# Optimization experiments

Hardware: AMD Instinct MI355X
Metric: run time of the kernel (lower is better)

The kernel has to match this reference:

```python
import jax, jax.numpy as jnp
import numpy as np

GRID = 7
NUM_CLASSES = 80
LAMBDA_COORD = 5.0
LAMBDA_NOOBJ = 0.5
EPS_IOU = 1e-06
EPS_SQRT = 1e-06


def setup_inputs() -> dict:
    key = jax.random.key(0)
    k1, k2, k3 = jax.random.split(key, 3)
    B = 4096
    D = 10 + NUM_CLASSES
    pred = jax.random.uniform(k1, (B, GRID, GRID, D), dtype=jnp.float32)
    target = jax.random.uniform(k2, (B, GRID, GRID, D), dtype=jnp.float32)
    # confidence channel of target must be exactly 1.0 for object cells
    obj = (jax.random.uniform(k3, (B, GRID, GRID)) < 0.25).astype(jnp.float32)
    target = target.at[..., 4].set(obj)
    return {"pred": pred, "target": target}


def _iou(b1, b2):
    # b1, b2: [..., 4] boxes as (cx, cy, w, h) in image coords
    x1, y1, w1, h1 = b1[..., 0], b1[..., 1], b1[..., 2], b1[..., 3]
    x2, y2, w2, h2 = b2[..., 0], b2[..., 1], b2[..., 2], b2[..., 3]
    ix_min = jnp.maximum(x1 - w1 / 2, x2 - w2 / 2)
    iy_min = jnp.maximum(y1 - h1 / 2, y2 - h2 / 2)
    ix_max = jnp.minimum(x1 + w1 / 2, x2 + w2 / 2)
    iy_max = jnp.minimum(y1 + h1 / 2, y2 + h2 / 2)
    iw = jnp.clip(ix_max - ix_min, 0.0)
    ih = jnp.clip(iy_max - iy_min, 0.0)
    inter = iw * ih
    union = w1 * h1 + w2 * h2 - inter
    return inter / (union + EPS_IOU)


def _forward(pred, target):
    S = pred.shape[1]
    gy = jnp.arange(S, dtype=pred.dtype).reshape(1, S, 1)
    gx = jnp.arange(S, dtype=pred.dtype).reshape(1, 1, S)

    def to_img(box5):  # [B,S,S,5] cell-relative -> [B,S,S,4] image coords
        cx = (gx + box5[..., 0]) / S
        cy = (gy + box5[..., 1]) / S
        return jnp.stack([cx, cy, box5[..., 2], box5[..., 3]], axis=-1)

    box1 = pred[..., 0:5]
    box2 = pred[..., 5:10]
    tbox = target[..., 0:5]

    iou1 = _iou(to_img(box1), to_img(tbox))
    iou2 = _iou(to_img(box2), to_img(tbox))
    resp1 = iou1 > iou2  # box1 responsible if strictly greater (matches `if iou1 > iou2`)
    best = jnp.where(resp1[..., None], box1, box2)  # [B,S,S,5]

    obj = target[..., 4] == 1.0  # [B,S,S]
    objf = obj.astype(pred.dtype)
    n_obj = jnp.sum(objf)
    n_cells = jnp.asarray(pred.shape[0] * S * S, pred.dtype)

    # coord: mean-of-2 xy MSE + mean-of-2 sqrt(wh) MSE per responsible box
    dxy2 = jnp.sum((best[..., 0:2] - tbox[..., 0:2]) ** 2, axis=-1)
    swh_p = jnp.sqrt(jnp.clip(best[..., 2:4], EPS_SQRT))
    swh_t = jnp.sqrt(jnp.clip(tbox[..., 2:4], EPS_SQRT))
    dwh2 = jnp.sum((swh_p - swh_t) ** 2, axis=-1)
    coord_per = 0.5 * dxy2 + 0.5 * dwh2
    coord_loss = jnp.sum(coord_per * objf) / jnp.maximum(n_obj, 1.0)

    # confidence: obj cells -> (best_conf - 1)^2 (count 1); noobj -> lam*(c1^2 + c2^2) (count 2)
    conf_obj = (best[..., 4] - 1.0) ** 2
    conf_noobj = LAMBDA_NOOBJ * (pred[..., 4] ** 2 + pred[..., 9] ** 2)
    conf_sum = jnp.sum(jnp.where(obj, conf_obj, conf_noobj))
    conf_count = n_obj + 2.0 * (n_cells - n_obj)
    conf_loss = conf_sum / jnp.maximum(conf_count, 1.0)

    # class: mean over classes per obj cell
    class_per = jnp.mean((pred[..., 10:] - target[..., 10:]) ** 2, axis=-1)
    class_loss = jnp.sum(class_per * objf) / jnp.maximum(n_obj, 1.0)

    return LAMBDA_COORD * coord_loss + conf_loss + class_loss


def reference(pred, target):
    return _forward(pred, target)
```

## Files before the change

kernel.cpp:

```cpp
#include <hip/hip_runtime.h>

#define GRID_S 7
#define NUM_CLASSES 80
#define D_DIM 90
#define LAMBDA_COORD 5.0f
#define LAMBDA_NOOBJ 0.5f
#define EPS_IOU 1e-6f
#define EPS_SQRT 1e-6f

__device__ __forceinline__ float iou_img(float cx1, float cy1, float w1, float h1,
                                         float cx2, float cy2, float w2, float h2) {
    float ixmin = fmaxf(cx1 - w1 * 0.5f, cx2 - w2 * 0.5f);
    float iymin = fmaxf(cy1 - h1 * 0.5f, cy2 - h2 * 0.5f);
    float ixmax = fminf(cx1 + w1 * 0.5f, cx2 + w2 * 0.5f);
    float iymax = fminf(cy1 + h1 * 0.5f, cy2 + h2 * 0.5f);
    float iw = fmaxf(ixmax - ixmin, 0.0f);
    float ih = fmaxf(iymax - iymin, 0.0f);
    float inter = iw * ih;
    float uni = w1 * h1 + w2 * h2 - inter;
    return inter / (uni + EPS_IOU);
}

__global__ __launch_bounds__(256) void yolo_gated_kernel(
        const float* __restrict__ pred, const float* __restrict__ targ,
        float* __restrict__ part, int ncells) {
    const int tid = threadIdx.x;
    const int cell = blockIdx.x * 256 + tid;

    __shared__ int s_list[256];
    __shared__ int s_count;
    if (tid == 0) s_count = 0;
    __syncthreads();

    float v_obj = 0.0f, v_coord = 0.0f, v_conf = 0.0f, v_cls = 0.0f;

    bool obj = false;
    if (cell < ncells) {
        const float2* t2 = (const float2*)(targ + (size_t)cell * D_DIM);
        const float2* p2 = (const float2*)(pred + (size_t)cell * D_DIM);
        float2 tf = t2[2];
        float2 pa = p2[2];
        float2 pb = p2[4];
        obj = (tf.x == 1.0f);
        if (obj) {
            v_obj = 1.0f;
        } else {
            v_conf = LAMBDA_NOOBJ * (pa.x * pa.x + pb.y * pb.y);
        }
    }

    if (obj) {
        int idx = atomicAdd(&s_count, 1);
        s_list[idx] = cell;
    }
    __syncthreads();
    const int n = s_count;

    const int lane6 = tid & 63;
    const int sub = tid >> 6;
    for (int k0 = 0; k0 < n; k0 += 64) {
        const int k = k0 + lane6;
        if (k < n) {
            const int c = s_list[k];
            const float2* p2 = (const float2*)(pred + (size_t)c * D_DIM);
            const float2* t2 = (const float2*)(targ + (size_t)c * D_DIM);

            float cls0 = 0.0f, cls1 = 0.0f;
            const int s2 = 5 + 10 * sub;
            #pragma unroll
            for (int j = 0; j < 10; ++j) {
                float2 pc = p2[s2 + j];
                float2 tc = t2[s2 + j];
                float dx = pc.x - tc.x;
                float dy = pc.y - tc.y;
                cls0 = fmaf(dx, dx, cls0);
                cls1 = fmaf(dy, dy, cls1);
            }
            v_cls += (cls0 + cls1) * (1.0f / (float)NUM_CLASSES);

            if (sub == 0) {
                float2 pq0 = p2[0], pq1 = p2[1], pq2 = p2[2], pq3 = p2[3], pq4 = p2[4];
                float2 tq0 = t2[0], tq1 = t2[1];

                float b1x = pq0.x, b1y = pq0.y, b1w = pq1.x, b1h = pq1.y, b1c = pq2.x;
                float b2x = pq2.y, b2y = pq3.x, b2w = pq3.y, b2h = pq4.x, b2c = pq4.y;
                float tbx = tq0.x, tby = tq0.y, tbw = tq1.x, tbh = tq1.y;

                const int gxy = c % (GRID_S * GRID_S);
                const float gy = (float)(gxy / GRID_S);
                const float gx = (float)(gxy % GRID_S);
                const float invS = 1.0f / (float)GRID_S;
                float c1x = (gx + b1x) * invS, c1y = (gy + b1y) * invS;
                float c2x = (gx + b2x) * invS, c2y = (gy + b2y) * invS;
                float ctx = (gx + tbx) * invS, cty = (gy + tby) * invS;

                float iou1 = iou_img(c1x, c1y, b1w, b1h, ctx, cty, tbw, tbh);
                float iou2 = iou_img(c2x, c2y, b2w, b2h, ctx, cty, tbw, tbh);
                bool resp1 = iou1 > iou2;

                float bx = resp1 ? b1x : b2x;
                float by = resp1 ? b1y : b2y;
                float bw = resp1 ? b1w : b2w;
                float bh = resp1 ? b1h : b2h;
                float bc = resp1 ? b1c : b2c;

                float ddx = bx - tbx, ddy = by - tby;
                float dxy2 = ddx * ddx + ddy * ddy;
                float swpw = sqrtf(fmaxf(bw, EPS_SQRT));
                float swph = sqrtf(fmaxf(bh, EPS_SQRT));
                float swtw = sqrtf(fmaxf(tbw, EPS_SQRT));
                float swth = sqrtf(fmaxf(tbh, EPS_SQRT));
                float dw = swpw - swtw, dh = swph - swth;
                float dwh2 = dw * dw + dh * dh;

                v_coord += 0.5f * dxy2 + 0.5f * dwh2;
                float dco = bc - 1.0f;
                v_conf += dco * dco;
            }
        }
    }

    #pragma unroll
    for (int off = 32; off > 0; off >>= 1) {
        v_obj   += __shfl_down(v_obj, off, 64);
        v_coord += __shfl_down(v_coord, off, 64);
        v_conf  += __shfl_down(v_conf, off, 64);
        v_cls   += __shfl_down(v_cls, off, 64);
    }
    __shared__ float red[4][4];
    const int lane = tid & 63;
    const int wid = tid >> 6;
    if (lane == 0) {
        red[wid][0] = v_obj;
        red[wid][1] = v_coord;
        red[wid][2] = v_conf;
        red[wid][3] = v_cls;
    }
    __syncthreads();
    if (tid < 4) {
        float s = red[0][tid] + red[1][tid] + red[2][tid] + red[3][tid];
        part[(size_t)blockIdx.x * 4 + tid] = s;
    }
}

__global__ __launch_bounds__(1024) void yolo_final_kernel(
        const float* __restrict__ part, float* __restrict__ out,
        int nblocks, int ncells) {
    const int tid = threadIdx.x;
    float a0 = 0.0f, a1 = 0.0f, a2 = 0.0f, a3 = 0.0f;
    const float4* p4 = (const float4*)part;
    for (int b = tid; b < nblocks; b += 1024) {
        float4 v = p4[b];
        a0 += v.x; a1 += v.y; a2 += v.z; a3 += v.w;
    }
    #pragma unroll
    for (int off = 32; off > 0; off >>= 1) {
        a0 += __shfl_down(a0, off, 64);
        a1 += __shfl_down(a1, off, 64);
        a2 += __shfl_down(a2, off, 64);
        a3 += __shfl_down(a3, off, 64);
    }
    __shared__ float red[16][4];
    const int wid = tid >> 6;
    if ((tid & 63) == 0) {
        red[wid][0] = a0; red[wid][1] = a1; red[wid][2] = a2; red[wid][3] = a3;
    }
    __syncthreads();
    if (tid == 0) {
        float n_obj = 0.0f, coord = 0.0f, conf = 0.0f, cls = 0.0f;
        #pragma unroll
        for (int w = 0; w < 16; ++w) {
            n_obj += red[w][0]; coord += red[w][1];
            conf  += red[w][2]; cls   += red[w][3];
        }
        float n_cells = (float)ncells;
        float conf_count = n_obj + 2.0f * (n_cells - n_obj);
        float denom = fmaxf(n_obj, 1.0f);
        out[0] = LAMBDA_COORD * coord / denom + conf / fmaxf(conf_count, 1.0f) + cls / denom;
    }
}

extern "C" void kernel_launch(void* const* d_in, const int* in_sizes, int n_in,
                              void* d_out, int out_size, void* d_ws, size_t ws_size,
                              hipStream_t stream) {
    const float* pred = (const float*)d_in[0];
    const float* targ = (const float*)d_in[1];
    float* part = (float*)d_ws;
    float* out = (float*)d_out;

    const int ncells = in_sizes[0] / D_DIM;
    const int nblocks = (ncells + 255) / 256;

    yolo_gated_kernel<<<nblocks, 256, 0, stream>>>(pred, targ, part, ncells);
    yolo_final_kernel<<<1, 1024, 0, stream>>>(part, out, nblocks, ncells);
}
```

Measured before the change: 151.8 us.

## Pair threads per cell, splitting flag and noobj reads across lanes

Each block now handles 128 cells with two threads per cell. One lane of each pair reads the target flag and appends object cells to the shared list, while its partner reads the two predicted confidences only for non-object cells. Object cells are then processed by thread pairs, each covering 40 class values through explicitly batched loads. Launch bounds now ask for 6 blocks per SM. The intent is more memory-level parallelism and more blocks for this sparse, latency-bound gather, at the cost of a shuffle and twice as many blocks.

New measurement: 167.3 us. 1.1x slower.

```diff
diff --git a/kernel.cpp b/kernel.cpp
--- a/kernel.cpp
+++ b/kernel.cpp
@@ -7,6 +7,8 @@
 #define LAMBDA_NOOBJ 0.5f
 #define EPS_IOU 1e-6f
 #define EPS_SQRT 1e-6f
+
+#define CPB 128
 
 __device__ __forceinline__ float iou_img(float cx1, float cy1, float w1, float h1,
                                          float cx2, float cy2, float w2, float h2) {
@@ -21,66 +23,80 @@
     return inter / (uni + EPS_IOU);
 }
 
-__global__ __launch_bounds__(256) void yolo_gated_kernel(
+__global__ __launch_bounds__(256, 6) void yolo_pair_kernel(
         const float* __restrict__ pred, const float* __restrict__ targ,
         float* __restrict__ part, int ncells) {
     const int tid = threadIdx.x;
-    const int cell = blockIdx.x * 256 + tid;
-
-    __shared__ int s_list[256];
+    const int lane = tid & 63;
+    const int pc = tid >> 1;
+    const int which = tid & 1;
+    const int cell = blockIdx.x * CPB + pc;
+    const bool cv = (cell < ncells);
+
+    __shared__ int s_list[CPB];
     __shared__ int s_count;
     if (tid == 0) s_count = 0;
     __syncthreads();
 
     float v_obj = 0.0f, v_coord = 0.0f, v_conf = 0.0f, v_cls = 0.0f;
 
-    bool obj = false;
-    if (cell < ncells) {
-        const float2* t2 = (const float2*)(targ + (size_t)cell * D_DIM);
-        const float2* p2 = (const float2*)(pred + (size_t)cell * D_DIM);
-        float2 tf = t2[2];
-        float2 pa = p2[2];
-        float2 pb = p2[4];
-        obj = (tf.x == 1.0f);
-        if (obj) {
+    const float2* p2 = (const float2*)(pred + (size_t)cell * D_DIM);
+    const float2* t2 = (const float2*)(targ + (size_t)cell * D_DIM);
+
+    float flagval = 0.0f;
+    if (cv && which) {
+        flagval = t2[2].x;
+    }
+    float pf = __shfl(flagval, lane ^ 1, 64);
+
+    if (which) {
+        bool obj = (flagval == 1.0f);
+        if (cv && obj) {
             v_obj = 1.0f;
-        } else {
+            int idx = atomicAdd(&s_count, 1);
+            s_list[idx] = cell;
+        }
+    } else {
+        bool obj = (pf == 1.0f);
+        if (cv && !obj) {
+            float2 pa = p2[2];
+            float2 pb = p2[4];
             v_conf = LAMBDA_NOOBJ * (pa.x * pa.x + pb.y * pb.y);
         }
     }
-
-    if (obj) {
-        int idx = atomicAdd(&s_count, 1);
-        s_list[idx] = cell;
-    }
     __syncthreads();
     const int n = s_count;
 
-    const int lane6 = tid & 63;
-    const int sub = tid >> 6;
-    for (int k0 = 0; k0 < n; k0 += 64) {
-        const int k = k0 + lane6;
+    for (int k0 = 0; k0 < n; k0 += CPB) {
+        const int k = k0 + pc;
         if (k < n) {
             const int c = s_list[k];
-            const float2* p2 = (const float2*)(pred + (size_t)c * D_DIM);
-            const float2* t2 = (const float2*)(targ + (size_t)c * D_DIM);
+            const float2* cp2 = (const float2*)(pred + (size_t)c * D_DIM);
+            const float2* ct2 = (const float2*)(targ + (size_t)c * D_DIM);
 
             float cls0 = 0.0f, cls1 = 0.0f;
-            const int s2 = 5 + 10 * sub;
+            const int jbase = 5 + 20 * which;
             #pragma unroll
-            for (int j = 0; j < 10; ++j) {
-                float2 pc = p2[s2 + j];
-                float2 tc = t2[s2 + j];
-                float dx = pc.x - tc.x;
-                float dy = pc.y - tc.y;
-                cls0 = fmaf(dx, dx, cls0);
-                cls1 = fmaf(dy, dy, cls1);
+            for (int j0 = 0; j0 < 20; j0 += 10) {
+                float2 P[10], T[10];
+                #pragma unroll
+                for (int j = 0; j < 10; ++j) {
+                    P[j] = cp2[jbase + j0 + j];
+                    T[j] = ct2[jbase + j0 + j];
+                }
+                #pragma unroll
+                for (int j = 0; j < 10; ++j) {
+                    float dx = P[j].x - T[j].x;
+                    float dy = P[j].y - T[j].y;
+                    cls0 = fmaf(dx, dx, cls0);
+                    cls1 = fmaf(dy, dy, cls1);
+                }
             }
             v_cls += (cls0 + cls1) * (1.0f / (float)NUM_CLASSES);
 
-            if (sub == 0) {
-                float2 pq0 = p2[0], pq1 = p2[1], pq2 = p2[2], pq3 = p2[3], pq4 = p2[4];
-                float2 tq0 = t2[0], tq1 = t2[1];
+            if (which == 0) {
+                float2 pq0 = cp2[0], pq1 = cp2[1], pq2 = cp2[2], pq3 = cp2[3], pq4 = cp2[4];
+                float2 tq0 = ct2[0], tq1 = ct2[1];
 
                 float b1x = pq0.x, b1y = pq0.y, b1w = pq1.x, b1h = pq1.y, b1c = pq2.x;
                 float b2x = pq2.y, b2y = pq3.x, b2w = pq3.y, b2h = pq4.x, b2c = pq4.y;
@@ -128,7 +144,6 @@
         v_cls   += __shfl_down(v_cls, off, 64);
     }
     __shared__ float red[4][4];
-    const int lane = tid & 63;
     const int wid = tid >> 6;
     if (lane == 0) {
         red[wid][0] = v_obj;
@@ -189,8 +204,8 @@
     float* out = (float*)d_out;
 
     const int ncells = in_sizes[0] / D_DIM;
-    const int nblocks = (ncells + 255) / 256;
-
-    yolo_gated_kernel<<<nblocks, 256, 0, stream>>>(pred, targ, part, ncells);
+    const int nblocks = (ncells + CPB - 1) / CPB;
+
+    yolo_pair_kernel<<<nblocks, 256, 0, stream>>>(pred, targ, part, ncells);
     yolo_final_kernel<<<1, 1024, 0, stream>>>(part, out, nblocks, ncells);
 }
```
